# Kernel tuning notes

Hardware: AMD Instinct MI355X
Metric: run time of the kernel (lower is better)

Reference implementation:

```python
import jax, jax.numpy as jnp
import numpy as np

EMBED_DIM = 1024
NUM_HEADS = 16
HEAD_DIM = EMBED_DIM // NUM_HEADS


def setup_inputs() -> dict:
    key = jax.random.key(0)
    ks = jax.random.split(key, 9)
    B, S, D = 1, 4096, EMBED_DIM
    scale = 1.0 / np.sqrt(D)
    x = jax.random.normal(ks[0], (B, S, D), dtype=jnp.float32)
    # Linear weights stored as [in, out]; torch nn.Linear init ~ U(-1/sqrt(in), 1/sqrt(in))
    wq = jax.random.uniform(ks[1], (D, D), jnp.float32, -scale, scale)
    bq = jax.random.uniform(ks[2], (D,), jnp.float32, -scale, scale)
    wk = jax.random.uniform(ks[3], (D, D), jnp.float32, -scale, scale)
    bk = jax.random.uniform(ks[4], (D,), jnp.float32, -scale, scale)
    wv = jax.random.uniform(ks[5], (D, D), jnp.float32, -scale, scale)
    bv = jax.random.uniform(ks[6], (D,), jnp.float32, -scale, scale)
    wo = jax.random.uniform(ks[7], (D, D), jnp.float32, -scale, scale)
    bo = jax.random.uniform(ks[8], (D,), jnp.float32, -scale, scale)
    return {"x": x, "wq": wq, "bq": bq, "wk": wk, "bk": bk,
            "wv": wv, "bv": bv, "wo": wo, "bo": bo}


def reference(x, wq, bq, wk, bk, wv, bv, wo, bo):
    B, S, D = x.shape
    H, Hd = NUM_HEADS, HEAD_DIM
    # QKV projections
    q = x @ wq + bq  # [B,S,D]
    k = x @ wk + bk
    v = x @ wv + bv
    # split heads -> [B,H,S,Hd]
    q = q.reshape(B, S, H, Hd).transpose(0, 2, 1, 3)
    k = k.reshape(B, S, H, Hd).transpose(0, 2, 1, 3)
    v = v.reshape(B, S, H, Hd).transpose(0, 2, 1, 3)
    inv_sqrt_d = 1.0 / np.sqrt(Hd).astype(np.float32)
    scores = jnp.einsum('bhqd,bhkd->bhqk', q, k) * inv_sqrt_d  # [B,H,S,S]
    attn = jax.nn.softmax(scores, axis=-1)
    out = jnp.einsum('bhqk,bhkd->bhqd', attn, v)  # [B,H,S,Hd]
    out = out.transpose(0, 2, 1, 3).reshape(B, S, D)
    return out @ wo + bo
```

## Files before the change

kernel.cpp:

```cpp
#include <hip/hip_runtime.h>

typedef unsigned short u16;
typedef unsigned int u32;
typedef short v8s __attribute__((ext_vector_type(8)));
typedef float f32x4 __attribute__((ext_vector_type(4)));
typedef float f32x16 __attribute__((ext_vector_type(16)));

#define S_LEN 4096
#define DM 1024
#define HDIM 64
#define CEXP 0.18033688f

__device__ __forceinline__ u16 f2bs(float f) {
  u32 u = __float_as_uint(f);
  u32 r = 0x7FFFu + ((u >> 16) & 1u);
  return (u16)((u + r) >> 16);
}

__device__ __forceinline__ float fexp2(float x) {
  float r;
  asm("v_exp_f32 %0, %1" : "=v"(r) : "v"(x));
  return r;
}

__device__ __forceinline__ void gstage16(const void* g, void* lds_wave_base) {
  __builtin_amdgcn_global_load_lds(
      (const __attribute__((address_space(1))) u32*)g,
      (__attribute__((address_space(3))) u32*)lds_wave_base, 16, 0, 0);
}

__device__ __forceinline__ f32x16 vzero16() {
  f32x16 v;
#pragma unroll
  for (int r = 0; r < 16; ++r) v[r] = 0.f;
  return v;
}

__global__ void k_cvt(const float* __restrict__ in, u16* __restrict__ out) {
  const int i = blockIdx.x * blockDim.x + threadIdx.x;
  const float4* p = reinterpret_cast<const float4*>(in) + (size_t)i * 2;
  float4 a = p[0], b = p[1];
  u16 t[8] = {f2bs(a.x), f2bs(a.y), f2bs(a.z), f2bs(a.w),
              f2bs(b.x), f2bs(b.y), f2bs(b.z), f2bs(b.w)};
  reinterpret_cast<uint4*>(out)[i] = *reinterpret_cast<const uint4*>(t);
}

__global__ __launch_bounds__(256) void k_wtrans(
    const float* __restrict__ w0, const float* __restrict__ w1,
    const float* __restrict__ w2, const float* __restrict__ w3,
    u16* __restrict__ t0, u16* __restrict__ t1,
    u16* __restrict__ t2, u16* __restrict__ t3) {
  __shared__ float tile[32][33];
  const float* w; u16* wt;
  switch (blockIdx.z) {
    case 0: w = w0; wt = t0; break;
    case 1: w = w1; wt = t1; break;
    case 2: w = w2; wt = t2; break;
    default: w = w3; wt = t3; break;
  }
  const int r = threadIdx.x >> 3;
  const int c4 = (threadIdx.x & 7) * 4;
  const int k0 = blockIdx.x * 32, n0 = blockIdx.y * 32;
  float4 v = *reinterpret_cast<const float4*>(w + (size_t)(k0 + r) * DM + n0 + c4);
  tile[r][c4] = v.x; tile[r][c4 + 1] = v.y; tile[r][c4 + 2] = v.z; tile[r][c4 + 3] = v.w;
  __syncthreads();
  u16 o4[4] = {f2bs(tile[c4][r]), f2bs(tile[c4 + 1][r]),
               f2bs(tile[c4 + 2][r]), f2bs(tile[c4 + 3][r])};
  *reinterpret_cast<uint2*>(wt + (size_t)(n0 + r) * DM + k0 + c4) =
      *reinterpret_cast<const uint2*>(o4);
}

template <int MODE>
__device__ __forceinline__ void gemm_core(
    u16* __restrict__ As, u16* __restrict__ Bs,
    const u16* __restrict__ A, const u16* __restrict__ Bt,
    const float* __restrict__ bias, void* __restrict__ Cout, float oscale) {
  constexpr int K = DM, N = DM;
  const int tid = threadIdx.x;
  const int lane = tid & 63, wave = tid >> 6;
  const int wm = wave >> 1, wn = wave & 1;
  const int l15 = lane & 15, l4 = lane >> 4;
  const int bm0 = blockIdx.x * 128, bn0 = blockIdx.y * 128;

  f32x4 acc[4][4];
#pragma unroll
  for (int m = 0; m < 4; ++m)
#pragma unroll
    for (int n = 0; n < 4; ++n) acc[m][n] = 0.f;

  const int s0 = tid, s1 = tid + 256;
  const int ra0 = s0 >> 2, ca0 = ((s0 & 3) ^ ((ra0 >> 1) & 3)) * 8;
  const int ra1 = s1 >> 2, ca1 = ((s1 & 3) ^ ((ra1 >> 1) & 3)) * 8;
  const u16* Ab = A + (size_t)bm0 * K;
  const u16* Bb = Bt + (size_t)bn0 * K;
  u16* ldsA0 = As + (size_t)(wave * 64) * 8;
  u16* ldsA1 = As + (size_t)(256 + wave * 64) * 8;
  u16* ldsB0 = Bs + (size_t)(wave * 64) * 8;
  u16* ldsB1 = Bs + (size_t)(256 + wave * 64) * 8;

  for (int k0 = 0; k0 < K; k0 += 32) {
    gstage16(Ab + (size_t)ra0 * K + k0 + ca0, ldsA0);
    gstage16(Ab + (size_t)ra1 * K + k0 + ca1, ldsA1);
    gstage16(Bb + (size_t)ra0 * K + k0 + ca0, ldsB0);
    gstage16(Bb + (size_t)ra1 * K + k0 + ca1, ldsB1);
    __syncthreads();
    v8s af[4], bfr[4];
#pragma unroll
    for (int m = 0; m < 4; ++m) {
      const int rowa = wm * 64 + m * 16 + l15;
      af[m] = *reinterpret_cast<const v8s*>(
          As + (size_t)(rowa * 4 + (l4 ^ ((rowa >> 1) & 3))) * 8);
      const int rowb = wn * 64 + m * 16 + l15;
      bfr[m] = *reinterpret_cast<const v8s*>(
          Bs + (size_t)(rowb * 4 + (l4 ^ ((rowb >> 1) & 3))) * 8);
    }
#pragma unroll
    for (int m = 0; m < 4; ++m)
#pragma unroll
      for (int n = 0; n < 4; ++n)
        acc[m][n] = __builtin_amdgcn_mfma_f32_16x16x32_bf16(af[m], bfr[n], acc[m][n], 0, 0, 0);
    __syncthreads();
  }

#pragma unroll
  for (int m = 0; m < 4; ++m) {
    const int gs0 = bm0 + wm * 64 + m * 16 + l4 * 4;
#pragma unroll
    for (int n = 0; n < 4; ++n) {
      const int gn = bn0 + wn * 64 + n * 16 + l15;
      const float bv = bias[gn];
      if (MODE == 0) {
        u16* O = (u16*)Cout;
        const size_t base = (size_t)(gn >> 6) * (S_LEN * HDIM) + (size_t)(gn & 63);
#pragma unroll
        for (int r = 0; r < 4; ++r)
          O[base + (size_t)(gs0 + r) * HDIM] = f2bs((acc[m][n][r] + bv) * oscale);
      } else if (MODE == 1) {
        u16* O = (u16*)Cout;
        u16 p4[4];
#pragma unroll
        for (int r = 0; r < 4; ++r) p4[r] = f2bs(acc[m][n][r] + bv);
        *reinterpret_cast<uint2*>(O + (size_t)(gn >> 6) * (HDIM * S_LEN) +
                                  (size_t)(gn & 63) * S_LEN + gs0) =
            *reinterpret_cast<const uint2*>(p4);
      } else {
        float* O = (float*)Cout;
#pragma unroll
        for (int r = 0; r < 4; ++r)
          O[(size_t)(gs0 + r) * N + gn] = acc[m][n][r] + bv;
      }
    }
  }
}

__global__ __launch_bounds__(256) void k_gemm_qkv(
    const u16* __restrict__ A,
    const u16* __restrict__ wq, const u16* __restrict__ wk, const u16* __restrict__ wv,
    const float* __restrict__ bq, const float* __restrict__ bk, const float* __restrict__ bv,
    u16* __restrict__ Qo, u16* __restrict__ Ko, u16* __restrict__ Vo) {
  __shared__ __attribute__((aligned(16))) u16 As[128 * 32];
  __shared__ __attribute__((aligned(16))) u16 Bs[128 * 32];
  const int z = blockIdx.z;
  if (z == 0)      gemm_core<0>(As, Bs, A, wq, bq, Qo, CEXP);
  else if (z == 1) gemm_core<0>(As, Bs, A, wk, bk, Ko, 1.f);
  else             gemm_core<1>(As, Bs, A, wv, bv, Vo, 1.f);
}

__global__ __launch_bounds__(256) void k_gemm_o(
    const u16* __restrict__ A, const u16* __restrict__ wo,
    const float* __restrict__ bo, float* __restrict__ out) {
  __shared__ __attribute__((aligned(16))) u16 As[128 * 32];
  __shared__ __attribute__((aligned(16))) u16 Bs[128 * 32];
  gemm_core<2>(As, Bs, A, wo, bo, out, 1.f);
}

__global__ __launch_bounds__(256, 2) void k_attn(
    const u16* __restrict__ Q, const u16* __restrict__ Kg,
    const u16* __restrict__ Vt, u16* __restrict__ Aout) {
  __shared__ __attribute__((aligned(16))) u16 Ks[3][64 * 64];
  __shared__ __attribute__((aligned(16))) u16 Vs[3][64 * 64];

  const int tid = threadIdx.x;
  const int lane = tid & 63, wave = tid >> 6;
  const int l31 = lane & 31, lh = lane >> 5;

  const int id = blockIdx.x;
  const int xcd = id & 7, sp = id >> 3;
  const int h = xcd * 2 + (sp & 1);
  const int qb = sp >> 1;
  const int q0 = qb * 128 + wave * 32;

  const u16* Qh = Q + (size_t)h * S_LEN * HDIM;
  const u16* Kh = Kg + (size_t)h * S_LEN * HDIM;
  const u16* Vh = Vt + (size_t)h * HDIM * S_LEN;

  v8s qf[4];
#pragma unroll
  for (int ks = 0; ks < 4; ++ks)
    qf[ks] = *reinterpret_cast<const v8s*>(
        Qh + (size_t)(q0 + l31) * HDIM + ks * 16 + lh * 8);

  const short ONE = 0x3F80;
  const v8s ones = {ONE, ONE, ONE, ONE, ONE, ONE, ONE, ONE};
  const f32x16 z16 = vzero16();

  f32x16 oacc[2], accl;
  oacc[0] = z16; oacc[1] = z16; accl = z16;

  const int s0i = tid, s1i = tid + 256;
  const int r0 = s0i >> 3, c0 = ((s0i & 7) ^ (r0 & 7)) * 8;
  const int r1 = s1i >> 3, c1 = ((s1i & 7) ^ (r1 & 7)) * 8;

  auto stageKV = [&](int b, int t) {
    const int kv0 = t * 64;
    gstage16(Kh + (size_t)(kv0 + r0) * HDIM + c0, &Ks[b][(wave * 64) * 8]);
    gstage16(Kh + (size_t)(kv0 + r1) * HDIM + c1, &Ks[b][(256 + wave * 64) * 8]);
    gstage16(Vh + (size_t)r0 * S_LEN + kv0 + c0, &Vs[b][(wave * 64) * 8]);
    gstage16(Vh + (size_t)r1 * S_LEN + kv0 + c1, &Vs[b][(256 + wave * 64) * 8]);
  };

  auto qk = [&](const u16* Kb, f32x16 (&sO)[2]) {
    __builtin_amdgcn_s_setprio(1);
#pragma unroll
    for (int j = 0; j < 2; ++j) {
      const int row = j * 32 + l31;
      v8s k0 = *reinterpret_cast<const v8s*>(
          Kb + (size_t)(row * 8 + ((0 + lh) ^ (row & 7))) * 8);
      sO[j] = __builtin_amdgcn_mfma_f32_32x32x16_bf16(k0, qf[0], z16, 0, 0, 0);
#pragma unroll
      for (int ks = 1; ks < 4; ++ks) {
        v8s kf = *reinterpret_cast<const v8s*>(
            Kb + (size_t)(row * 8 + ((ks * 2 + lh) ^ (row & 7))) * 8);
        sO[j] = __builtin_amdgcn_mfma_f32_32x32x16_bf16(kf, qf[ks], sO[j], 0, 0, 0);
      }
    }
    __builtin_amdgcn_s_setprio(0);
  };

  auto body = [&](int t, int ib, f32x16 (&sIn)[2], f32x16 (&sOut)[2],
                  bool hasNext, bool hasNext2) {
    asm volatile("s_waitcnt vmcnt(0)\n\ts_barrier" ::: "memory");
    if (hasNext2) stageKV(ib == 0 ? 2 : ib - 1, t + 2);
    if (hasNext) qk(&Ks[ib == 2 ? 0 : ib + 1][0], sOut);

    const u16* Vb = &Vs[ib][0];
    v8s vf[2][4];
#pragma unroll
    for (int n = 0; n < 2; ++n) {
      const int row = n * 32 + l31;
#pragma unroll
      for (int ks = 0; ks < 4; ++ks)
        vf[n][ks] = *reinterpret_cast<const v8s*>(
            Vb + (size_t)(row * 8 + ((ks * 2 + lh) ^ (row & 7))) * 8);
    }

    v8s pf[4];
#pragma unroll
    for (int j = 0; j < 2; ++j) {
      float p[16];
#pragma unroll
      for (int r = 0; r < 16; ++r) p[r] = fexp2(sIn[j][r]);
      u32 X1, X2, X3, X4, Y1, Y2, Y3, Y4;
      asm("v_cvt_pk_bf16_f32 %0, %1, %2" : "=v"(X1) : "v"(p[0]), "v"(p[1]));
      asm("v_cvt_pk_bf16_f32 %0, %1, %2" : "=v"(Y1) : "v"(p[4]), "v"(p[5]));
      asm("v_cvt_pk_bf16_f32 %0, %1, %2" : "=v"(X2) : "v"(p[2]), "v"(p[3]));
      asm("v_cvt_pk_bf16_f32 %0, %1, %2" : "=v"(Y2) : "v"(p[6]), "v"(p[7]));
      asm("v_cvt_pk_bf16_f32 %0, %1, %2" : "=v"(X3) : "v"(p[8]), "v"(p[9]));
      asm("v_cvt_pk_bf16_f32 %0, %1, %2" : "=v"(Y3) : "v"(p[12]), "v"(p[13]));
      asm("v_cvt_pk_bf16_f32 %0, %1, %2" : "=v"(X4) : "v"(p[10]), "v"(p[11]));
      asm("v_cvt_pk_bf16_f32 %0, %1, %2" : "=v"(Y4) : "v"(p[14]), "v"(p[15]));
      asm("v_permlane32_swap_b32 %0, %1" : "+v"(X1), "+v"(Y1));
      asm("v_permlane32_swap_b32 %0, %1" : "+v"(X2), "+v"(Y2));
      asm("v_permlane32_swap_b32 %0, %1" : "+v"(X3), "+v"(Y3));
      asm("v_permlane32_swap_b32 %0, %1" : "+v"(X4), "+v"(Y4));
      uint4 w0; w0.x = X1; w0.y = X2; w0.z = Y1; w0.w = Y2;
      uint4 w1; w1.x = X3; w1.y = X4; w1.z = Y3; w1.w = Y4;
      pf[j * 2 + 0] = *reinterpret_cast<const v8s*>(&w0);
      pf[j * 2 + 1] = *reinterpret_cast<const v8s*>(&w1);
    }

    __builtin_amdgcn_s_setprio(1);
#pragma unroll
    for (int ks = 0; ks < 4; ++ks) {
      accl = __builtin_amdgcn_mfma_f32_32x32x16_bf16(pf[ks], ones, accl, 0, 0, 0);
      oacc[0] = __builtin_amdgcn_mfma_f32_32x32x16_bf16(pf[ks], vf[0][ks], oacc[0], 0, 0, 0);
      oacc[1] = __builtin_amdgcn_mfma_f32_32x32x16_bf16(pf[ks], vf[1][ks], oacc[1], 0, 0, 0);
    }
    __builtin_amdgcn_s_setprio(0);
  };

  constexpr int NT = S_LEN / 64;
  f32x16 sacc0[2], sacc1[2];

  stageKV(0, 0);
  stageKV(1, 1);
  asm volatile("s_waitcnt vmcnt(4)\n\ts_barrier" ::: "memory");
  qk(&Ks[0][0], sacc0);

  int ib = 0;
  for (int tt = 0; tt < NT - 2; tt += 2) {
    body(tt, ib, sacc0, sacc1, true, true);
    const int ib1 = (ib == 2) ? 0 : ib + 1;
    body(tt + 1, ib1, sacc1, sacc0, true, true);
    ib += 2; if (ib >= 3) ib -= 3;
  }
  body(NT - 2, ib, sacc0, sacc1, true, false);
  const int ibL = (ib == 2) ? 0 : ib + 1;
  body(NT - 1, ibL, sacc1, sacc0, false, false);

#pragma unroll
  for (int r = 0; r < 16; ++r) {
    const float inv = __builtin_amdgcn_rcpf(accl[r]);
    const int q = q0 + (r & 3) + 8 * (r >> 2) + 4 * lh;
    const size_t base = (size_t)q * DM + h * HDIM + l31;
    Aout[base] = f2bs(oacc[0][r] * inv);
    Aout[base + 32] = f2bs(oacc[1][r] * inv);
  }
}

extern "C" void kernel_launch(void* const* d_in, const int* in_sizes, int n_in,
                              void* d_out, int out_size, void* d_ws, size_t ws_size,
                              hipStream_t stream) {
  const float* x  = (const float*)d_in[0];
  const float* wq = (const float*)d_in[1];
  const float* bq = (const float*)d_in[2];
  const float* wk = (const float*)d_in[3];
  const float* bk = (const float*)d_in[4];
  const float* wv = (const float*)d_in[5];
  const float* bv = (const float*)d_in[6];
  const float* wo = (const float*)d_in[7];
  const float* bo = (const float*)d_in[8];
  float* out = (float*)d_out;

  char* ws = (char*)d_ws;
  u16* xb  = (u16*)(ws);
  u16* wqT = (u16*)(ws + (8u << 20));
  u16* wkT = wqT + 1024 * 1024;
  u16* wvT = wkT + 1024 * 1024;
  u16* woT = wvT + 1024 * 1024;
  u16* Qh  = (u16*)(ws + (16u << 20));
  u16* Kh  = Qh + 16 * 4096 * 64;
  u16* Vth = Kh + 16 * 4096 * 64;
  u16* Ao  = Vth + 16 * 4096 * 64;

  k_cvt<<<2048, 256, 0, stream>>>(x, xb);
  dim3 tg(32, 32, 4);
  k_wtrans<<<tg, 256, 0, stream>>>(wq, wk, wv, wo, wqT, wkT, wvT, woT);
  dim3 gg(32, 8, 3);
  k_gemm_qkv<<<gg, 256, 0, stream>>>(xb, wqT, wkT, wvT, bq, bk, bv, Qh, Kh, Vth);
  k_attn<<<512, 256, 0, stream>>>(Qh, Kh, Vth, Ao);
  dim3 og(32, 8);
  k_gemm_o<<<og, 256, 0, stream>>>(Ao, woT, bo, out);
}
```

Baseline: 167.7 us.

## Split attention KV range across two blocks and reduce partial outputs

```diff
diff --git a/kernel.cpp b/kernel.cpp
--- a/kernel.cpp
+++ b/kernel.cpp
@@ -174,11 +174,12 @@
   gemm_core<2>(As, Bs, A, wo, bo, out, 1.f);
 }
 
-__global__ __launch_bounds__(256, 2) void k_attn(
+__global__ __launch_bounds__(256, 4) void k_attn_split(
     const u16* __restrict__ Q, const u16* __restrict__ Kg,
-    const u16* __restrict__ Vt, u16* __restrict__ Aout) {
-  __shared__ __attribute__((aligned(16))) u16 Ks[3][64 * 64];
-  __shared__ __attribute__((aligned(16))) u16 Vs[3][64 * 64];
+    const u16* __restrict__ Vt, float* __restrict__ Po0,
+    float* __restrict__ Po1, float* __restrict__ Pl) {
+  __shared__ __attribute__((aligned(16))) u16 Ks[2][64 * 64];
+  __shared__ __attribute__((aligned(16))) u16 Vs[2][64 * 64];
 
   const int tid = threadIdx.x;
   const int lane = tid & 63, wave = tid >> 6;
@@ -187,8 +188,10 @@
   const int id = blockIdx.x;
   const int xcd = id & 7, sp = id >> 3;
   const int h = xcd * 2 + (sp & 1);
-  const int qb = sp >> 1;
+  const int qb = (sp >> 1) & 31;
+  const int hh = sp >> 6;
   const int q0 = qb * 128 + wave * 32;
+  const int bt = hh * 32;
 
   const u16* Qh = Q + (size_t)h * S_LEN * HDIM;
   const u16* Kh = Kg + (size_t)h * S_LEN * HDIM;
@@ -211,10 +214,13 @@
   const int r0 = s0i >> 3, c0 = ((s0i & 7) ^ (r0 & 7)) * 8;
   const int r1 = s1i >> 3, c1 = ((s1i & 7) ^ (r1 & 7)) * 8;
 
-  auto stageKV = [&](int b, int t) {
-    const int kv0 = t * 64;
+  auto stageK = [&](int b, int gt) {
+    const int kv0 = gt * 64;
     gstage16(Kh + (size_t)(kv0 + r0) * HDIM + c0, &Ks[b][(wave * 64) * 8]);
     gstage16(Kh + (size_t)(kv0 + r1) * HDIM + c1, &Ks[b][(256 + wave * 64) * 8]);
+  };
+  auto stageV = [&](int b, int gt) {
+    const int kv0 = gt * 64;
     gstage16(Vh + (size_t)r0 * S_LEN + kv0 + c0, &Vs[b][(wave * 64) * 8]);
     gstage16(Vh + (size_t)r1 * S_LEN + kv0 + c1, &Vs[b][(256 + wave * 64) * 8]);
   };
@@ -237,13 +243,14 @@
     __builtin_amdgcn_s_setprio(0);
   };
 
-  auto body = [&](int t, int ib, f32x16 (&sIn)[2], f32x16 (&sOut)[2],
-                  bool hasNext, bool hasNext2) {
+  auto body = [&](int j, int par, f32x16 (&sIn)[2], f32x16 (&sOut)[2],
+                  bool k2, bool n1) {
     asm volatile("s_waitcnt vmcnt(0)\n\ts_barrier" ::: "memory");
-    if (hasNext2) stageKV(ib == 0 ? 2 : ib - 1, t + 2);
-    if (hasNext) qk(&Ks[ib == 2 ? 0 : ib + 1][0], sOut);
-
-    const u16* Vb = &Vs[ib][0];
+    if (k2) stageK(par, bt + j + 2);
+    if (n1) stageV(par ^ 1, bt + j + 1);
+    if (n1) qk(&Ks[par ^ 1][0], sOut);
+
+    const u16* Vb = &Vs[par][0];
     v8s vf[2][4];
 #pragma unroll
     for (int n = 0; n < 2; ++n) {
@@ -256,10 +263,10 @@
 
     v8s pf[4];
 #pragma unroll
-    for (int j = 0; j < 2; ++j) {
+    for (int jj = 0; jj < 2; ++jj) {
       float p[16];
 #pragma unroll
-      for (int r = 0; r < 16; ++r) p[r] = fexp2(sIn[j][r]);
+      for (int r = 0; r < 16; ++r) p[r] = fexp2(sIn[jj][r]);
       u32 X1, X2, X3, X4, Y1, Y2, Y3, Y4;
       asm("v_cvt_pk_bf16_f32 %0, %1, %2" : "=v"(X1) : "v"(p[0]), "v"(p[1]));
       asm("v_cvt_pk_bf16_f32 %0, %1, %2" : "=v"(Y1) : "v"(p[4]), "v"(p[5]));
@@ -275,8 +282,171 @@
       asm("v_permlane32_swap_b32 %0, %1" : "+v"(X4), "+v"(Y4));
       uint4 w0; w0.x = X1; w0.y = X2; w0.z = Y1; w0.w = Y2;
       uint4 w1; w1.x = X3; w1.y = X4; w1.z = Y3; w1.w = Y4;
-      pf[j * 2 + 0] = *reinterpret_cast<const v8s*>(&w0);
-      pf[j * 2 + 1] = *reinterpret_cast<const v8s*>(&w1);
+      pf[jj * 2 + 0] = *reinterpret_cast<const v8s*>(&w0);
+      pf[jj * 2 + 1] = *reinterpret_cast<const v8s*>(&w1);
+    }
+
+    __builtin_amdgcn_s_setprio(1);
+#pragma unroll
+    for (int ks = 0; ks < 4; ++ks) {
+      accl = __builtin_amdgcn_mfma_f32_32x32x16_bf16(pf[ks], ones, accl, 0, 0, 0);
+      oacc[0] = __builtin_amdgcn_mfma_f32_32x32x16_bf16(pf[ks], vf[0][ks], oacc[0], 0, 0, 0);
+      oacc[1] = __builtin_amdgcn_mfma_f32_32x32x16_bf16(pf[ks], vf[1][ks], oacc[1], 0, 0, 0);
+    }
+    __builtin_amdgcn_s_setprio(0);
+  };
+
+  f32x16 sacc0[2], sacc1[2];
+
+  stageK(0, bt);
+  stageK(1, bt + 1);
+  stageV(0, bt);
+  asm volatile("s_waitcnt vmcnt(4)\n\ts_barrier" ::: "memory");
+  qk(&Ks[0][0], sacc0);
+
+  for (int j = 0; j < 30; j += 2) {
+    body(j, 0, sacc0, sacc1, true, true);
+    body(j + 1, 1, sacc1, sacc0, true, true);
+  }
+  body(30, 0, sacc0, sacc1, false, true);
+  body(31, 1, sacc1, sacc0, false, false);
+
+  float* Po = hh ? Po1 : Po0;
+  float* Plh = Pl + (size_t)hh * 16 * S_LEN + (size_t)h * S_LEN;
+#pragma unroll
+  for (int r = 0; r < 16; ++r) {
+    const int q = q0 + (r & 3) + 8 * (r >> 2) + 4 * lh;
+    const size_t base = (size_t)q * DM + h * HDIM + l31;
+    Po[base] = oacc[0][r];
+    Po[base + 32] = oacc[1][r];
+    if (l31 == 0) Plh[q] = accl[r];
+  }
+}
+
+__global__ __launch_bounds__(256) void k_reduce(
+    const float* __restrict__ Po0, const float* __restrict__ Po1,
+    const float* __restrict__ Pl, u16* __restrict__ Ao) {
+  const int idx = blockIdx.x * 256 + threadIdx.x;
+  const int q = idx >> 7;
+  const int c8 = (idx & 127) << 3;
+  const int h = c8 >> 6;
+  const float l = Pl[(size_t)h * S_LEN + q] +
+                  Pl[(size_t)16 * S_LEN + (size_t)h * S_LEN + q];
+  const float inv = 1.f / l;
+  const size_t base = (size_t)q * DM + c8;
+  const float4* a = reinterpret_cast<const float4*>(Po0 + base);
+  const float4* b = reinterpret_cast<const float4*>(Po1 + base);
+  float4 a0 = a[0], a1 = a[1], b0 = b[0], b1 = b[1];
+  u16 t[8] = {f2bs((a0.x + b0.x) * inv), f2bs((a0.y + b0.y) * inv),
+              f2bs((a0.z + b0.z) * inv), f2bs((a0.w + b0.w) * inv),
+              f2bs((a1.x + b1.x) * inv), f2bs((a1.y + b1.y) * inv),
+              f2bs((a1.z + b1.z) * inv), f2bs((a1.w + b1.w) * inv)};
+  *reinterpret_cast<uint4*>(Ao + base) = *reinterpret_cast<const uint4*>(t);
+}
+
+__global__ __launch_bounds__(256, 2) void k_attn(
+    const u16* __restrict__ Q, const u16* __restrict__ Kg,
+    const u16* __restrict__ Vt, u16* __restrict__ Aout) {
+  __shared__ __attribute__((aligned(16))) u16 Ks[3][64 * 64];
+  __shared__ __attribute__((aligned(16))) u16 Vs[3][64 * 64];
+
+  const int tid = threadIdx.x;
+  const int lane = tid & 63, wave = tid >> 6;
+  const int l31 = lane & 31, lh = lane >> 5;
+
+  const int id = blockIdx.x;
+  const int xcd = id & 7, sp = id >> 3;
+  const int h = xcd * 2 + (sp & 1);
+  const int qb = sp >> 1;
+  const int q0 = qb * 128 + wave * 32;
+
+  const u16* Qh = Q + (size_t)h * S_LEN * HDIM;
+  const u16* Kh = Kg + (size_t)h * S_LEN * HDIM;
+  const u16* Vh = Vt + (size_t)h * HDIM * S_LEN;
+
+  v8s qf[4];
+#pragma unroll
+  for (int ks = 0; ks < 4; ++ks)
+    qf[ks] = *reinterpret_cast<const v8s*>(
+        Qh + (size_t)(q0 + l31) * HDIM + ks * 16 + lh * 8);
+
+  const short ONE = 0x3F80;
+  const v8s ones = {ONE, ONE, ONE, ONE, ONE, ONE, ONE, ONE};
+  const f32x16 z16 = vzero16();
+
+  f32x16 oacc[2], accl;
+  oacc[0] = z16; oacc[1] = z16; accl = z16;
+
+  const int s0i = tid, s1i = tid + 256;
+  const int r0 = s0i >> 3, c0 = ((s0i & 7) ^ (r0 & 7)) * 8;
+  const int r1 = s1i >> 3, c1 = ((s1i & 7) ^ (r1 & 7)) * 8;
+
+  auto stageKV = [&](int b, int t) {
+    const int kv0 = t * 64;
+    gstage16(Kh + (size_t)(kv0 + r0) * HDIM + c0, &Ks[b][(wave * 64) * 8]);
+    gstage16(Kh + (size_t)(kv0 + r1) * HDIM + c1, &Ks[b][(256 + wave * 64) * 8]);
+    gstage16(Vh + (size_t)r0 * S_LEN + kv0 + c0, &Vs[b][(wave * 64) * 8]);
+    gstage16(Vh + (size_t)r1 * S_LEN + kv0 + c1, &Vs[b][(256 + wave * 64) * 8]);
+  };
+
+  auto qk = [&](const u16* Kb, f32x16 (&sO)[2]) {
+    __builtin_amdgcn_s_setprio(1);
+#pragma unroll
+    for (int j = 0; j < 2; ++j) {
+      const int row = j * 32 + l31;
+      v8s k0 = *reinterpret_cast<const v8s*>(
+          Kb + (size_t)(row * 8 + ((0 + lh) ^ (row & 7))) * 8);
+      sO[j] = __builtin_amdgcn_mfma_f32_32x32x16_bf16(k0, qf[0], z16, 0, 0, 0);
+#pragma unroll
+      for (int ks = 1; ks < 4; ++ks) {
+        v8s kf = *reinterpret_cast<const v8s*>(
+            Kb + (size_t)(row * 8 + ((ks * 2 + lh) ^ (row & 7))) * 8);
+        sO[j] = __builtin_amdgcn_mfma_f32_32x32x16_bf16(kf, qf[ks], sO[j], 0, 0, 0);
+      }
+    }
+    __builtin_amdgcn_s_setprio(0);
+  };
+
+  auto body = [&](int t, int ib, f32x16 (&sIn)[2], f32x16 (&sOut)[2],
+                  bool hasNext, bool hasNext2) {
+    asm volatile("s_waitcnt vmcnt(0)\n\ts_barrier" ::: "memory");
+    if (hasNext2) stageKV(ib == 0 ? 2 : ib - 1, t + 2);
+    if (hasNext) qk(&Ks[ib == 2 ? 0 : ib + 1][0], sOut);
+
+    const u16* Vb = &Vs[ib][0];
+    v8s vf[2][4];
+#pragma unroll
+    for (int n = 0; n < 2; ++n) {
+      const int row = n * 32 + l31;
+#pragma unroll
+      for (int ks = 0; ks < 4; ++ks)
+        vf[n][ks] = *reinterpret_cast<const v8s*>(
+            Vb + (size_t)(row * 8 + ((ks * 2 + lh) ^ (row & 7))) * 8);
+    }
+
+    v8s pf[4];
+#pragma unroll
+    for (int jj = 0; jj < 2; ++jj) {
+      float p[16];
+#pragma unroll
+      for (int r = 0; r < 16; ++r) p[r] = fexp2(sIn[jj][r]);
+      u32 X1, X2, X3, X4, Y1, Y2, Y3, Y4;
+      asm("v_cvt_pk_bf16_f32 %0, %1, %2" : "=v"(X1) : "v"(p[0]), "v"(p[1]));
+      asm("v_cvt_pk_bf16_f32 %0, %1, %2" : "=v"(Y1) : "v"(p[4]), "v"(p[5]));
+      asm("v_cvt_pk_bf16_f32 %0, %1, %2" : "=v"(X2) : "v"(p[2]), "v"(p[3]));
+      asm("v_cvt_pk_bf16_f32 %0, %1, %2" : "=v"(Y2) : "v"(p[6]), "v"(p[7]));
+      asm("v_cvt_pk_bf16_f32 %0, %1, %2" : "=v"(X3) : "v"(p[8]), "v"(p[9]));
+      asm("v_cvt_pk_bf16_f32 %0, %1, %2" : "=v"(Y3) : "v"(p[12]), "v"(p[13]));
+      asm("v_cvt_pk_bf16_f32 %0, %1, %2" : "=v"(X4) : "v"(p[10]), "v"(p[11]));
+      asm("v_cvt_pk_bf16_f32 %0, %1, %2" : "=v"(Y4) : "v"(p[14]), "v"(p[15]));
+      asm("v_permlane32_swap_b32 %0, %1" : "+v"(X1), "+v"(Y1));
+      asm("v_permlane32_swap_b32 %0, %1" : "+v"(X2), "+v"(Y2));
+      asm("v_permlane32_swap_b32 %0, %1" : "+v"(X3), "+v"(Y3));
+      asm("v_permlane32_swap_b32 %0, %1" : "+v"(X4), "+v"(Y4));
+      uint4 w0; w0.x = X1; w0.y = X2; w0.z = Y1; w0.w = Y2;
+      uint4 w1; w1.x = X3; w1.y = X4; w1.z = Y3; w1.w = Y4;
+      pf[jj * 2 + 0] = *reinterpret_cast<const v8s*>(&w0);
+      pf[jj * 2 + 1] = *reinterpret_cast<const v8s*>(&w1);
     }
 
     __builtin_amdgcn_s_setprio(1);
@@ -342,13 +512,21 @@
   u16* Kh  = Qh + 16 * 4096 * 64;
   u16* Vth = Kh + 16 * 4096 * 64;
   u16* Ao  = Vth + 16 * 4096 * 64;
+  float* Po1 = (float*)(ws + (48u << 20));
+  float* Pl  = (float*)(ws + (64u << 20));
+  const bool split = ws_size >= ((64u << 20) + (1u << 20));
 
   k_cvt<<<2048, 256, 0, stream>>>(x, xb);
   dim3 tg(32, 32, 4);
   k_wtrans<<<tg, 256, 0, stream>>>(wq, wk, wv, wo, wqT, wkT, wvT, woT);
   dim3 gg(32, 8, 3);
   k_gemm_qkv<<<gg, 256, 0, stream>>>(xb, wqT, wkT, wvT, bq, bk, bv, Qh, Kh, Vth);
-  k_attn<<<512, 256, 0, stream>>>(Qh, Kh, Vth, Ao);
+  if (split) {
+    k_attn_split<<<1024, 256, 0, stream>>>(Qh, Kh, Vth, out, Po1, Pl);
+    k_reduce<<<2048, 256, 0, stream>>>(out, Po1, Pl, Ao);
+  } else {
+    k_attn<<<512, 256, 0, stream>>>(Qh, Kh, Vth, Ao);
+  }
   dim3 og(32, 8);
   k_gemm_o<<<og, 256, 0, stream>>>(Ao, woT, bo, out);
 }
```

Result: slower. 669.7 us (+299.3%).

## Process two KV tiles per barrier with four-slot LDS buffering in attention

Applied to the files above, without the earlier changes.

```diff
diff --git a/kernel.cpp b/kernel.cpp
--- a/kernel.cpp
+++ b/kernel.cpp
@@ -177,8 +177,8 @@
 __global__ __launch_bounds__(256, 2) void k_attn(
     const u16* __restrict__ Q, const u16* __restrict__ Kg,
     const u16* __restrict__ Vt, u16* __restrict__ Aout) {
-  __shared__ __attribute__((aligned(16))) u16 Ks[3][64 * 64];
-  __shared__ __attribute__((aligned(16))) u16 Vs[3][64 * 64];
+  __shared__ __attribute__((aligned(16))) u16 Ks[4][64 * 64];
+  __shared__ __attribute__((aligned(16))) u16 Vs[4][64 * 64];
 
   const int tid = threadIdx.x;
   const int lane = tid & 63, wave = tid >> 6;
@@ -237,13 +237,7 @@
     __builtin_amdgcn_s_setprio(0);
   };
 
-  auto body = [&](int t, int ib, f32x16 (&sIn)[2], f32x16 (&sOut)[2],
-                  bool hasNext, bool hasNext2) {
-    asm volatile("s_waitcnt vmcnt(0)\n\ts_barrier" ::: "memory");
-    if (hasNext2) stageKV(ib == 0 ? 2 : ib - 1, t + 2);
-    if (hasNext) qk(&Ks[ib == 2 ? 0 : ib + 1][0], sOut);
-
-    const u16* Vb = &Vs[ib][0];
+  auto halfTile = [&](const u16* Vb, f32x16 (&sIn)[2]) {
     v8s vf[2][4];
 #pragma unroll
     for (int n = 0; n < 2; ++n) {
@@ -256,10 +250,10 @@
 
     v8s pf[4];
 #pragma unroll
-    for (int j = 0; j < 2; ++j) {
+    for (int jj = 0; jj < 2; ++jj) {
       float p[16];
 #pragma unroll
-      for (int r = 0; r < 16; ++r) p[r] = fexp2(sIn[j][r]);
+      for (int r = 0; r < 16; ++r) p[r] = fexp2(sIn[jj][r]);
       u32 X1, X2, X3, X4, Y1, Y2, Y3, Y4;
       asm("v_cvt_pk_bf16_f32 %0, %1, %2" : "=v"(X1) : "v"(p[0]), "v"(p[1]));
       asm("v_cvt_pk_bf16_f32 %0, %1, %2" : "=v"(Y1) : "v"(p[4]), "v"(p[5]));
@@ -275,8 +269,8 @@
       asm("v_permlane32_swap_b32 %0, %1" : "+v"(X4), "+v"(Y4));
       uint4 w0; w0.x = X1; w0.y = X2; w0.z = Y1; w0.w = Y2;
       uint4 w1; w1.x = X3; w1.y = X4; w1.z = Y3; w1.w = Y4;
-      pf[j * 2 + 0] = *reinterpret_cast<const v8s*>(&w0);
-      pf[j * 2 + 1] = *reinterpret_cast<const v8s*>(&w1);
+      pf[jj * 2 + 0] = *reinterpret_cast<const v8s*>(&w0);
+      pf[jj * 2 + 1] = *reinterpret_cast<const v8s*>(&w1);
     }
 
     __builtin_amdgcn_s_setprio(1);
@@ -289,24 +283,26 @@
     __builtin_amdgcn_s_setprio(0);
   };
 
-  constexpr int NT = S_LEN / 64;
   f32x16 sacc0[2], sacc1[2];
+
+  auto body2 = [&](int t, int b0, int b1, int b2, int b3, bool doStage) {
+    asm volatile("s_waitcnt vmcnt(0)\n\ts_barrier" ::: "memory");
+    if (doStage) { stageKV(b2, t + 2); stageKV(b3, t + 3); }
+    qk(&Ks[b0][0], sacc0);
+    qk(&Ks[b1][0], sacc1);
+    halfTile(&Vs[b0][0], sacc0);
+    halfTile(&Vs[b1][0], sacc1);
+  };
 
   stageKV(0, 0);
   stageKV(1, 1);
-  asm volatile("s_waitcnt vmcnt(4)\n\ts_barrier" ::: "memory");
-  qk(&Ks[0][0], sacc0);
-
-  int ib = 0;
-  for (int tt = 0; tt < NT - 2; tt += 2) {
-    body(tt, ib, sacc0, sacc1, true, true);
-    const int ib1 = (ib == 2) ? 0 : ib + 1;
-    body(tt + 1, ib1, sacc1, sacc0, true, true);
-    ib += 2; if (ib >= 3) ib -= 3;
-  }
-  body(NT - 2, ib, sacc0, sacc1, true, false);
-  const int ibL = (ib == 2) ? 0 : ib + 1;
-  body(NT - 1, ibL, sacc1, sacc0, false, false);
+
+  for (int tt = 0; tt < 60; tt += 4) {
+    body2(tt, 0, 1, 2, 3, true);
+    body2(tt + 2, 2, 3, 0, 1, true);
+  }
+  body2(60, 0, 1, 2, 3, true);
+  body2(62, 2, 3, 0, 1, false);
 
 #pragma unroll
   for (int r = 0; r < 16; ++r) {
```

Measured after the change: 159.6 us. -4.8%, faster.
